# Kernel tuning notes

Measured on AMD Instinct MI355X. Metric: run time of the kernel, lower is better.

## Reference

```python
import jax, jax.numpy as jnp
import numpy as np

B, T, DM, DK, TOPK, NGRAM = 8, 4096, 1024, 256, 4, 3


def setup_inputs() -> dict:
    key = jax.random.key(0)
    k0, k1, k2, k3 = jax.random.split(key, 4)
    std = np.sqrt(2.0 / (DM + DK)).astype(np.float32)
    query = jax.random.normal(k0, (B, T, DM), jnp.float32)
    key_t = jax.random.normal(k1, (B, T, DM), jnp.float32)
    wq = jax.random.normal(k2, (DK, DM), jnp.float32) * std
    wk = jax.random.normal(k3, (DK, DM), jnp.float32) * std
    bq = jnp.zeros((DK,), jnp.float32)
    bk = jnp.zeros((DK,), jnp.float32)
    # Structured mask: each query row keeps exactly TOPK consecutive key columns
    # (required by the module's masked_select -> view(batch, -1, topk)).
    starts = np.minimum(np.arange(T), T - TOPK)
    cols = starts[:, None] + np.arange(TOPK)[None, :]  # [T, TOPK], ascending
    m = np.ones((T, T), dtype=bool)
    m[np.arange(T)[:, None], cols] = False  # False = unmasked
    mask = jnp.asarray(m)[None]  # [1, T, T]
    return {"query": query, "key": key_t, "mask": mask,
            "wq": wq, "bq": bq, "wk": wk, "bk": bk,
            "topk": TOPK, "ngram": NGRAM}


def reference(query, key, mask, wq, bq, wk, bk, topk, ngram):
    # Projections (torch Linear: x @ W.T + b)
    q = jnp.einsum('btm,dm->btd', query, wq) + bq  # [B,T,DK]
    k = jnp.einsum('btm,dm->btd', key, wk) + bk    # [B,T,DK]
    attn = jax.nn.sigmoid(jnp.einsum('btd,bsd->bts', q, k) / 256.0)  # [B,T,T]
    # masked_select of the topk unmasked entries per row, in ascending column
    # order (matches torch row-major masked_select). argsort of bool puts
    # False (unmasked) columns first, stably, i.e. in ascending column order.
    idx = jnp.argsort(mask, axis=-1)[..., :topk]           # [Bm,T,topk]
    idx = jnp.broadcast_to(idx, attn.shape[:2] + (topk,))  # [B,T,topk]
    sp = jnp.take_along_axis(attn, idx, axis=-1)           # [B,T,topk]
    Bsz = sp.shape[0]
    tt = topk * topk
    # init block: [B,topk,topk] -> repeat along new axis -> [B,1,topk,topk*topk]
    sp_init = jnp.tile(sp[:, :topk, :][:, :, None, :], (1, 1, topk, 1)).reshape(Bsz, 1, topk, tt)
    # end block: repeat each element topk times along last axis
    sp_end = jnp.tile(sp[:, -topk:, :][..., None], (1, 1, 1, topk)).reshape(Bsz, 1, topk, tt)
    # middle n-gram blocks
    mid = sp[:, topk:-topk, :].reshape(Bsz, -1, topk, ngram - 1, topk)  # [B,G,topk,2,topk]
    before = mid[:, :, :, 0, :]  # [B,G,topk,topk]
    after = mid[:, :, :, 1, :]   # [B,G,topk,topk]
    sm = jnp.einsum('bgti,bgtj->bgtij', before, after).reshape(Bsz, -1, topk, tt)
    score_matrix = jnp.concatenate([sp_init, sm, sp_end], axis=1)  # [B,G+2,topk,tt]
    return score_matrix.sum(axis=-1)  # [B, G+2, topk]
```

## Files before the change

### kernel.cpp

```cpp
#include <hip/hip_runtime.h>
#include <hip/hip_bf16.h>
#include <stdint.h>

#define B_ 8
#define T_ 4096
#define DM_ 1024
#define DK_ 256

typedef __attribute__((ext_vector_type(8))) short short8;
typedef __attribute__((ext_vector_type(4))) float f32x4;
typedef __attribute__((ext_vector_type(4))) unsigned short ushort4v;
typedef __attribute__((ext_vector_type(8))) unsigned short ushort8v;

__device__ inline float bf2f(unsigned short u) {
    union { unsigned int u; float f; } v; v.u = ((unsigned int)u) << 16; return v.f;
}
__device__ inline unsigned short f2bf(float f) {
    __hip_bfloat16 h = __float2bfloat16(f);
    return __builtin_bit_cast(unsigned short, h);
}

__device__ inline void gload_lds16(const void* g, void* l) {
    __builtin_amdgcn_global_load_lds(
        (const __attribute__((address_space(1))) unsigned int*)g,
        (__attribute__((address_space(3))) unsigned int*)l, 16, 0, 0);
}

__global__ __launch_bounds__(256) void convw_kernel(
    const float* __restrict__ Wq, const float* __restrict__ Wk,
    unsigned short* __restrict__ Wpk)
{
    int t = blockIdx.x * 256 + threadIdx.x;
    int lane = t & 63;
    int n    = (t >> 6) & 15;
    int kt   = (t >> 10) & 31;
    int M    = t >> 15;
    const float* W = M ? Wk : Wq;
    int row = n * 16 + (lane & 15);
    int k0  = kt * 32 + (lane >> 4) * 8;
    const float* src = W + (size_t)row * DM_ + k0;
    f32x4 v0 = *(const f32x4*)(src);
    f32x4 v1 = *(const f32x4*)(src + 4);
    ushort8v u;
#pragma unroll
    for (int e = 0; e < 4; ++e) { u[e] = f2bf(v0[e]); u[e + 4] = f2bf(v1[e]); }
    *(ushort8v*)(Wpk + (size_t)t * 8) = u;
}

__global__ __launch_bounds__(512, 4) void proj_kernel(
    const float* __restrict__ Aq, const float* __restrict__ Ak,
    const unsigned short* __restrict__ Wpk,
    const float* __restrict__ bq, const float* __restrict__ bk,
    unsigned short* __restrict__ Oq, unsigned short* __restrict__ Ok)
{
    __shared__ __align__(16) char smem[2][32 * 1024];

    const bool isK = (blockIdx.z != 0);
    const float* A = isK ? Ak : Aq;
    const unsigned short* Wp = Wpk + (isK ? (size_t)32 * 16 * 64 * 8 : 0);
    const float* bias = isK ? bk : bq;
    unsigned short* O = isK ? Ok : Oq;

    const int row0 = blockIdx.x * 128;
    const int tid  = threadIdx.x;
    const int w    = tid >> 6;
    const int lane = tid & 63;
    const int lr   = lane & 15;
    const int lq   = lane >> 4;
    const int wr   = (w >> 2) * 64;
    const int wc   = (w & 3);

    const int arow = lane >> 3;
    const int aslt = (lane & 7) ^ (lane >> 3);

    f32x4 acc[4][4];
#pragma unroll
    for (int m = 0; m < 4; ++m)
#pragma unroll
        for (int n = 0; n < 4; ++n) acc[m][n] = (f32x4){0.f, 0.f, 0.f, 0.f};

#define STAGE(KT, BUF) {                                               \
    char* Ab_ = smem[BUF];                                             \
    char* Wb_ = smem[BUF] + 16 * 1024;                                 \
    const unsigned short* ws_ = Wp + (size_t)(KT) * 8192 + lane * 8;   \
    _Pragma("unroll")                                                  \
    for (int i_ = 0; i_ < 2; ++i_) {                                   \
        int c_ = w * 2 + i_;                                \
        int ra_ = c_ * 8 + arow;                     \
        gload_lds16(A + (size_t)(row0 + ra_) * DM_ + (KT) * 32         \
                      + aslt * 4,                                      \
                    Ab_ + c_ * 1024);                                  \
        gload_lds16(ws_ + (size_t)c_ * 1024 / 2 * 0 + c_ * 512,        \
                    Wb_ + c_ * 1024);                                  \
    } }

    STAGE(0, 0);

    for (int kt = 0; kt < 32; ++kt) {
        const int cur = kt & 1;
        if (kt < 31) {
            STAGE(kt + 1, cur ^ 1);
            asm volatile("s_waitcnt vmcnt(4)" ::: "memory");
        } else {
            asm volatile("s_waitcnt vmcnt(0)" ::: "memory");
        }
        __builtin_amdgcn_s_barrier();

        const char* As = smem[cur];
        const char* Ws = smem[cur] + 16 * 1024;

        short8 bF[4];
#pragma unroll
        for (int n = 0; n < 4; ++n)
            bF[n] = *(const short8*)(Ws + (wc * 4 + n) * 1024 + lane * 16);

#pragma unroll
        for (int m = 0; m < 4; ++m) {
            const int r = wr + m * 16 + lr;
            f32x4 a0 = *(const f32x4*)(As + r * 128 + (((lq * 2)     ^ (r & 7)) << 4));
            f32x4 a1 = *(const f32x4*)(As + r * 128 + (((lq * 2 + 1) ^ (r & 7)) << 4));
            short8 aF;
#pragma unroll
            for (int e = 0; e < 4; ++e) {
                aF[e]     = (short)f2bf(a0[e]);
                aF[e + 4] = (short)f2bf(a1[e]);
            }
#pragma unroll
            for (int n = 0; n < 4; ++n)
                acc[m][n] = __builtin_amdgcn_mfma_f32_16x16x32_bf16(
                    bF[n], aF, acc[m][n], 0, 0, 0);
        }
        asm volatile("s_waitcnt lgkmcnt(0)" ::: "memory");
        __builtin_amdgcn_s_barrier();
    }
#undef STAGE

#pragma unroll
    for (int m = 0; m < 4; ++m) {
        unsigned short* Orow = O + (size_t)(row0 + wr + m * 16 + lr) * DK_;
#pragma unroll
        for (int n = 0; n < 4; ++n) {
            const int col = (wc * 4 + n) * 16 + lq * 4;
            f32x4 bv = *(const f32x4*)(bias + col);
            ushort4v ov;
#pragma unroll
            for (int r4 = 0; r4 < 4; ++r4) ov[r4] = f2bf(acc[m][n][r4] + bv[r4]);
            *(ushort4v*)(Orow + col) = ov;
        }
    }
}

__global__ __launch_bounds__(256) void score_kernel(
    const unsigned short* __restrict__ Q, const unsigned short* __restrict__ K,
    float* __restrict__ S)
{
    constexpr int RS = 264;
    __shared__ unsigned short qs[64 * RS];
    __shared__ unsigned short ks[68 * RS];

    const int t0  = blockIdx.x * 64;
    const int b   = blockIdx.y;
    const int tid = threadIdx.x;

#pragma unroll
    for (int j = 0; j < 8; ++j) {
        int idx = j * 256 + tid;
        int r = idx >> 5, c = idx & 31;
        ushort8v v = *(const ushort8v*)(Q + ((size_t)(b * T_ + t0 + r)) * DK_ + c * 8);
        *(ushort8v*)(qs + r * RS + c * 8) = v;
    }
#pragma unroll
    for (int j = 0; j < 9; ++j) {
        int idx = j * 256 + tid;
        if (idx < 68 * 32) {
            int r = idx >> 5, c = idx & 31;
            int gr = t0 + r; if (gr > T_ - 1) gr = T_ - 1;
            ushort8v v = *(const ushort8v*)(K + ((size_t)(b * T_ + gr)) * DK_ + c * 8);
            *(ushort8v*)(ks + r * RS + c * 8) = v;
        }
    }
    __syncthreads();

    const int tl = tid >> 2;
    const int i  = tid & 3;
    const int t  = t0 + tl;
    int s = t; if (s > T_ - 4) s = T_ - 4;
    const int kl = s - t0 + i;

    const ushort8v* qr = (const ushort8v*)(qs + tl * RS);
    const ushort8v* kr = (const ushort8v*)(ks + kl * RS);
    float acc = 0.f;
#pragma unroll
    for (int d8 = 0; d8 < 32; ++d8) {
        ushort8v a = qr[d8], bb = kr[d8];
#pragma unroll
        for (int e = 0; e < 8; ++e) acc += bf2f(a[e]) * bf2f(bb[e]);
    }
    float sig = 1.0f / (1.0f + __expf(-acc * (1.0f / 256.0f)));
    sig += __shfl_xor(sig, 1);
    sig += __shfl_xor(sig, 2);
    if (i == 0) S[(size_t)b * T_ + t] = sig;
}

__global__ void out_kernel(const float* __restrict__ S, float* __restrict__ out)
{
    int idx = blockIdx.x * 256 + threadIdx.x;
    if (idx >= B_ * 513 * 4) return;
    int r = idx & 3;
    int g = (idx >> 2) % 513;
    int b = idx / (513 * 4);
    const float* Sb = S + (size_t)b * T_;
    float v;
    if (g == 0)        v = 4.0f * Sb[r];
    else if (g == 512) v = 4.0f * Sb[T_ - 4 + r];
    else { int base = 4 + (g - 1) * 8 + r * 2; v = Sb[base] * Sb[base + 1]; }
    out[idx] = v;
}

extern "C" void kernel_launch(void* const* d_in, const int* in_sizes, int n_in,
                              void* d_out, int out_size, void* d_ws, size_t ws_size,
                              hipStream_t stream)
{
    const float* query = (const float*)d_in[0];
    const float* key   = (const float*)d_in[1];
    const float* wq = (const float*)d_in[3];
    const float* bq = (const float*)d_in[4];
    const float* wk = (const float*)d_in[5];
    const float* bk = (const float*)d_in[6];
    float* out = (float*)d_out;

    unsigned short* Qb  = (unsigned short*)d_ws;
    unsigned short* Kb  = Qb + (size_t)B_ * T_ * DK_;
    float*          Sb  = (float*)(Kb + (size_t)B_ * T_ * DK_);
    unsigned short* Wpk = (unsigned short*)(Sb + (size_t)B_ * T_);

    hipLaunchKernelGGL(convw_kernel, dim3(256), dim3(256), 0, stream, wq, wk, Wpk);

    dim3 g1(B_ * T_ / 128, 1, 2);
    hipLaunchKernelGGL(proj_kernel, g1, dim3(512), 0, stream,
                       query, key, Wpk, bq, bk, Qb, Kb);

    dim3 g2(T_ / 64, B_);
    hipLaunchKernelGGL(score_kernel, g2, dim3(256), 0, stream, Qb, Kb, Sb);

    int tot = B_ * 513 * 4;
    hipLaunchKernelGGL(out_kernel, dim3((tot + 255) / 256), dim3(256), 0, stream, Sb, out);
}
```

Measured before the change: 85.76 us.

## Split projection GEMM into 128x128 output tiles with K=64 single-buffered stages

Changes the projection kernel from 512-thread blocks covering all 256 output columns to 256-thread blocks covering 128 columns, doubling the grid along y. Each k-iteration now stages a 64-wide K slice with a 16-slot XOR swizzle and uses __syncthreads instead of double-buffering with manual waitcnt. The packed weight layout in convw is reordered to match. The aim is more blocks and occupancy with fewer iterations, but the A input is now read twice (once per column half) and load/compute overlap within a block is lost.

```diff
diff --git a/kernel.cpp b/kernel.cpp
--- a/kernel.cpp
+++ b/kernel.cpp
@@ -32,12 +32,15 @@
 {
     int t = blockIdx.x * 256 + threadIdx.x;
     int lane = t & 63;
-    int n    = (t >> 6) & 15;
-    int kt   = (t >> 10) & 31;
+    int n    = (t >> 6) & 3;
+    int w2   = (t >> 8) & 1;
+    int kk   = (t >> 9) & 1;
+    int kt   = (t >> 10) & 15;
+    int y    = (t >> 14) & 1;
     int M    = t >> 15;
     const float* W = M ? Wk : Wq;
-    int row = n * 16 + (lane & 15);
-    int k0  = kt * 32 + (lane >> 4) * 8;
+    int row = y * 128 + w2 * 64 + n * 16 + (lane & 15);
+    int k0  = kt * 64 + kk * 32 + (lane >> 4) * 8;
     const float* src = W + (size_t)row * DM_ + k0;
     f32x4 v0 = *(const f32x4*)(src);
     f32x4 v1 = *(const f32x4*)(src + 4);
@@ -47,31 +50,33 @@
     *(ushort8v*)(Wpk + (size_t)t * 8) = u;
 }
 
-__global__ __launch_bounds__(512, 4) void proj_kernel(
+__global__ __launch_bounds__(256, 3) void proj_kernel(
     const float* __restrict__ Aq, const float* __restrict__ Ak,
     const unsigned short* __restrict__ Wpk,
     const float* __restrict__ bq, const float* __restrict__ bk,
     unsigned short* __restrict__ Oq, unsigned short* __restrict__ Ok)
 {
-    __shared__ __align__(16) char smem[2][32 * 1024];
+    __shared__ __align__(16) char smem[48 * 1024];
+    char* As = smem;
+    char* Ws = smem + 32 * 1024;
 
     const bool isK = (blockIdx.z != 0);
     const float* A = isK ? Ak : Aq;
-    const unsigned short* Wp = Wpk + (isK ? (size_t)32 * 16 * 64 * 8 : 0);
+    const unsigned short* Wp = Wpk
+        + (isK ? (size_t)262144 : 0)
+        + (size_t)blockIdx.y * 131072;
     const float* bias = isK ? bk : bq;
     unsigned short* O = isK ? Ok : Oq;
 
     const int row0 = blockIdx.x * 128;
+    const int col0 = blockIdx.y * 128;
     const int tid  = threadIdx.x;
     const int w    = tid >> 6;
     const int lane = tid & 63;
     const int lr   = lane & 15;
     const int lq   = lane >> 4;
-    const int wr   = (w >> 2) * 64;
-    const int wc   = (w & 3);
-
-    const int arow = lane >> 3;
-    const int aslt = (lane & 7) ^ (lane >> 3);
+    const int wr   = (w >> 1) * 64;
+    const int wch  = (w & 1);
 
     f32x4 acc[4][4];
 #pragma unroll
@@ -79,68 +84,54 @@
 #pragma unroll
         for (int n = 0; n < 4; ++n) acc[m][n] = (f32x4){0.f, 0.f, 0.f, 0.f};
 
-#define STAGE(KT, BUF) {                                               \
-    char* Ab_ = smem[BUF];                                             \
-    char* Wb_ = smem[BUF] + 16 * 1024;                                 \
-    const unsigned short* ws_ = Wp + (size_t)(KT) * 8192 + lane * 8;   \
-    _Pragma("unroll")                                                  \
-    for (int i_ = 0; i_ < 2; ++i_) {                                   \
-        int c_ = w * 2 + i_;                                \
-        int ra_ = c_ * 8 + arow;                     \
-        gload_lds16(A + (size_t)(row0 + ra_) * DM_ + (KT) * 32         \
-                      + aslt * 4,                                      \
-                    Ab_ + c_ * 1024);                                  \
-        gload_lds16(ws_ + (size_t)c_ * 1024 / 2 * 0 + c_ * 512,        \
-                    Wb_ + c_ * 1024);                                  \
-    } }
-
-    STAGE(0, 0);
-
-    for (int kt = 0; kt < 32; ++kt) {
-        const int cur = kt & 1;
-        if (kt < 31) {
-            STAGE(kt + 1, cur ^ 1);
-            asm volatile("s_waitcnt vmcnt(4)" ::: "memory");
-        } else {
-            asm volatile("s_waitcnt vmcnt(0)" ::: "memory");
-        }
-        __builtin_amdgcn_s_barrier();
-
-        const char* As = smem[cur];
-        const char* Ws = smem[cur] + 16 * 1024;
-
-        short8 bF[4];
-#pragma unroll
-        for (int n = 0; n < 4; ++n)
-            bF[n] = *(const short8*)(Ws + (wc * 4 + n) * 1024 + lane * 16);
-
-#pragma unroll
-        for (int m = 0; m < 4; ++m) {
-            const int r = wr + m * 16 + lr;
-            f32x4 a0 = *(const f32x4*)(As + r * 128 + (((lq * 2)     ^ (r & 7)) << 4));
-            f32x4 a1 = *(const f32x4*)(As + r * 128 + (((lq * 2 + 1) ^ (r & 7)) << 4));
-            short8 aF;
-#pragma unroll
-            for (int e = 0; e < 4; ++e) {
-                aF[e]     = (short)f2bf(a0[e]);
-                aF[e + 4] = (short)f2bf(a1[e]);
+    for (int kt = 0; kt < 16; ++kt) {
+#pragma unroll
+        for (int i = 0; i < 8; ++i) {
+            int idx = i * 256 + tid;
+            int r = idx >> 4, s = idx & 15;
+            gload_lds16(A + (size_t)(row0 + r) * DM_ + kt * 64 + ((s ^ (r & 15)) << 2),
+                        As + idx * 16);
+        }
+#pragma unroll
+        for (int i = 0; i < 4; ++i) {
+            int idx = i * 256 + tid;
+            gload_lds16(Wp + (size_t)kt * 8192 + idx * 8, Ws + idx * 16);
+        }
+        __syncthreads();
+
+#pragma unroll
+        for (int kk = 0; kk < 2; ++kk) {
+            short8 bF[4];
+#pragma unroll
+            for (int n = 0; n < 4; ++n)
+                bF[n] = *(const short8*)(Ws + ((kk * 2 + wch) * 4 + n) * 1024 + lane * 16);
+#pragma unroll
+            for (int m = 0; m < 4; ++m) {
+                const int r = wr + m * 16 + lr;
+                const int sb = kk * 8 + lq * 2;
+                f32x4 a0 = *(const f32x4*)(As + r * 256 + (((sb)     ^ lr) << 4));
+                f32x4 a1 = *(const f32x4*)(As + r * 256 + (((sb + 1) ^ lr) << 4));
+                short8 aF;
+#pragma unroll
+                for (int e = 0; e < 4; ++e) {
+                    aF[e]     = (short)f2bf(a0[e]);
+                    aF[e + 4] = (short)f2bf(a1[e]);
+                }
+#pragma unroll
+                for (int n = 0; n < 4; ++n)
+                    acc[m][n] = __builtin_amdgcn_mfma_f32_16x16x32_bf16(
+                        bF[n], aF, acc[m][n], 0, 0, 0);
             }
-#pragma unroll
-            for (int n = 0; n < 4; ++n)
-                acc[m][n] = __builtin_amdgcn_mfma_f32_16x16x32_bf16(
-                    bF[n], aF, acc[m][n], 0, 0, 0);
-        }
-        asm volatile("s_waitcnt lgkmcnt(0)" ::: "memory");
-        __builtin_amdgcn_s_barrier();
-    }
-#undef STAGE
+        }
+        __syncthreads();
+    }
 
 #pragma unroll
     for (int m = 0; m < 4; ++m) {
         unsigned short* Orow = O + (size_t)(row0 + wr + m * 16 + lr) * DK_;
 #pragma unroll
         for (int n = 0; n < 4; ++n) {
-            const int col = (wc * 4 + n) * 16 + lq * 4;
+            const int col = col0 + wch * 64 + n * 16 + lq * 4;
             f32x4 bv = *(const f32x4*)(bias + col);
             ushort4v ov;
 #pragma unroll
@@ -236,8 +227,8 @@
 
     hipLaunchKernelGGL(convw_kernel, dim3(256), dim3(256), 0, stream, wq, wk, Wpk);
 
-    dim3 g1(B_ * T_ / 128, 1, 2);
-    hipLaunchKernelGGL(proj_kernel, g1, dim3(512), 0, stream,
+    dim3 g1(B_ * T_ / 128, 2, 2);
+    hipLaunchKernelGGL(proj_kernel, g1, dim3(256), 0, stream,
                        query, key, Wpk, bq, bk, Qb, Kb);
 
     dim3 g2(T_ / 64, B_);
```

Measured after the change: 102.7 us. +19.7%, slower.

## Convert A tiles to bf16 in registers before LDS and fuse output kernel

Applied to the files above, without the earlier changes.

The projection kernel now loads fp32 activations into registers, converts them to bf16 once per thread, and writes bf16 tiles to LDS. This halves the LDS footprint for A and removes the repeated per-wave conversion of the same data, while the weights keep using direct global-to-LDS loads. It also adds s_setprio around the MFMA block, lowers launch bounds occupancy to 2, and folds the output n-gram assembly into the score kernel through a shuffle, dropping one launch and the S buffer. The risk is that register-staged A loads are less latency tolerant than async LDS loads.

```diff
diff --git a/kernel.cpp b/kernel.cpp
--- a/kernel.cpp
+++ b/kernel.cpp
@@ -47,17 +47,17 @@
     *(ushort8v*)(Wpk + (size_t)t * 8) = u;
 }
 
-__global__ __launch_bounds__(512, 4) void proj_kernel(
+__global__ __launch_bounds__(512, 2) void proj_kernel(
     const float* __restrict__ Aq, const float* __restrict__ Ak,
     const unsigned short* __restrict__ Wpk,
     const float* __restrict__ bq, const float* __restrict__ bk,
     unsigned short* __restrict__ Oq, unsigned short* __restrict__ Ok)
 {
-    __shared__ __align__(16) char smem[2][32 * 1024];
+    __shared__ __align__(16) char smem[2][24576];
 
     const bool isK = (blockIdx.z != 0);
     const float* A = isK ? Ak : Aq;
-    const unsigned short* Wp = Wpk + (isK ? (size_t)32 * 16 * 64 * 8 : 0);
+    const unsigned short* Wp = Wpk + (isK ? (size_t)262144 : 0);
     const float* bias = isK ? bk : bq;
     unsigned short* O = isK ? Ok : Oq;
 
@@ -68,10 +68,12 @@
     const int lr   = lane & 15;
     const int lq   = lane >> 4;
     const int wr   = (w >> 2) * 64;
-    const int wc   = (w & 3);
-
-    const int arow = lane >> 3;
-    const int aslt = (lane & 7) ^ (lane >> 3);
+    const int wc   = w & 3;
+
+    const int srow = tid >> 2;
+    const int schk = tid & 3;
+    const float* Asrc = A + (size_t)(row0 + srow) * DM_ + schk * 8;
+    const int awaddr = srow * 64 + ((schk ^ (srow & 3)) << 4);
 
     f32x4 acc[4][4];
 #pragma unroll
@@ -79,61 +81,60 @@
 #pragma unroll
         for (int n = 0; n < 4; ++n) acc[m][n] = (f32x4){0.f, 0.f, 0.f, 0.f};
 
-#define STAGE(KT, BUF) {                                               \
-    char* Ab_ = smem[BUF];                                             \
-    char* Wb_ = smem[BUF] + 16 * 1024;                                 \
-    const unsigned short* ws_ = Wp + (size_t)(KT) * 8192 + lane * 8;   \
-    _Pragma("unroll")                                                  \
-    for (int i_ = 0; i_ < 2; ++i_) {                                   \
-        int c_ = w * 2 + i_;                                \
-        int ra_ = c_ * 8 + arow;                     \
-        gload_lds16(A + (size_t)(row0 + ra_) * DM_ + (KT) * 32         \
-                      + aslt * 4,                                      \
-                    Ab_ + c_ * 1024);                                  \
-        gload_lds16(ws_ + (size_t)c_ * 1024 / 2 * 0 + c_ * 512,        \
-                    Wb_ + c_ * 1024);                                  \
-    } }
-
-    STAGE(0, 0);
+    f32x4 av0, av1;
+
+#define LOADA(KT) { const float* p_ = Asrc + (KT) * 32;            \
+                    av0 = *(const f32x4*)(p_);                      \
+                    av1 = *(const f32x4*)(p_ + 4); }
+#define STAGEW(KT, BUF) {                                           \
+    const unsigned short* ws_ = Wp + (size_t)(KT) * 8192;           \
+    gload_lds16(ws_ + (size_t)tid * 8,          smem[BUF] + 8192  + tid * 16); \
+    gload_lds16(ws_ + (size_t)(tid + 512) * 8,  smem[BUF] + 16384 + tid * 16); }
+#define CVTWRITE(BUF) {                                             \
+    ushort8v u_;                                                    \
+    _Pragma("unroll")                                               \
+    for (int e_ = 0; e_ < 4; ++e_) {                                \
+        u_[e_]     = f2bf(av0[e_]);                                 \
+        u_[e_ + 4] = f2bf(av1[e_]);                                 \
+    }                                                               \
+    *(ushort8v*)(smem[BUF] + awaddr) = u_; }
+
+    STAGEW(0, 0);
+    LOADA(0);
+    CVTWRITE(0);
+    __syncthreads();
 
     for (int kt = 0; kt < 32; ++kt) {
         const int cur = kt & 1;
         if (kt < 31) {
-            STAGE(kt + 1, cur ^ 1);
-            asm volatile("s_waitcnt vmcnt(4)" ::: "memory");
-        } else {
-            asm volatile("s_waitcnt vmcnt(0)" ::: "memory");
-        }
-        __builtin_amdgcn_s_barrier();
+            STAGEW(kt + 1, cur ^ 1);
+            LOADA(kt + 1);
+        }
 
         const char* As = smem[cur];
-        const char* Ws = smem[cur] + 16 * 1024;
-
+        const char* Ws = smem[cur] + 8192;
+        __builtin_amdgcn_s_setprio(1);
         short8 bF[4];
 #pragma unroll
         for (int n = 0; n < 4; ++n)
-            bF[n] = *(const short8*)(Ws + (wc * 4 + n) * 1024 + lane * 16);
-
+            bF[n] = *(const short8*)(Ws + ((wc * 4 + n) << 10) + (lane << 4));
 #pragma unroll
         for (int m = 0; m < 4; ++m) {
             const int r = wr + m * 16 + lr;
-            f32x4 a0 = *(const f32x4*)(As + r * 128 + (((lq * 2)     ^ (r & 7)) << 4));
-            f32x4 a1 = *(const f32x4*)(As + r * 128 + (((lq * 2 + 1) ^ (r & 7)) << 4));
-            short8 aF;
-#pragma unroll
-            for (int e = 0; e < 4; ++e) {
-                aF[e]     = (short)f2bf(a0[e]);
-                aF[e + 4] = (short)f2bf(a1[e]);
-            }
+            short8 aF = *(const short8*)(As + r * 64 + ((lq ^ (lr & 3)) << 4));
 #pragma unroll
             for (int n = 0; n < 4; ++n)
                 acc[m][n] = __builtin_amdgcn_mfma_f32_16x16x32_bf16(
                     bF[n], aF, acc[m][n], 0, 0, 0);
         }
-        asm volatile("s_waitcnt lgkmcnt(0)" ::: "memory");
-        __builtin_amdgcn_s_barrier();
-    }
-#undef STAGE
+        __builtin_amdgcn_s_setprio(0);
+
+        if (kt < 31) CVTWRITE(cur ^ 1);
+        __syncthreads();
+    }
+#undef LOADA
+#undef STAGEW
+#undef CVTWRITE
 
 #pragma unroll
     for (int m = 0; m < 4; ++m) {
@@ -152,7 +153,7 @@
 
 __global__ __launch_bounds__(256) void score_kernel(
     const unsigned short* __restrict__ Q, const unsigned short* __restrict__ K,
-    float* __restrict__ S)
+    float* __restrict__ out)
 {
     constexpr int RS = 264;
     __shared__ unsigned short qs[64 * RS];
@@ -199,22 +200,22 @@
     float sig = 1.0f / (1.0f + __expf(-acc * (1.0f / 256.0f)));
     sig += __shfl_xor(sig, 1);
     sig += __shfl_xor(sig, 2);
-    if (i == 0) S[(size_t)b * T_ + t] = sig;
-}
-
-__global__ void out_kernel(const float* __restrict__ S, float* __restrict__ out)
-{
-    int idx = blockIdx.x * 256 + threadIdx.x;
-    if (idx >= B_ * 513 * 4) return;
-    int r = idx & 3;
-    int g = (idx >> 2) % 513;
-    int b = idx / (513 * 4);
-    const float* Sb = S + (size_t)b * T_;
-    float v;
-    if (g == 0)        v = 4.0f * Sb[r];
-    else if (g == 512) v = 4.0f * Sb[T_ - 4 + r];
-    else { int base = 4 + (g - 1) * 8 + r * 2; v = Sb[base] * Sb[base + 1]; }
-    out[idx] = v;
+    float Snext = __shfl_xor(sig, 4);
+
+    if (i == 0) {
+        float* ob = out + (size_t)b * (513 * 4);
+        if (t < 4) {
+            ob[t] = 4.0f * sig;
+        } else if (t >= T_ - 4) {
+            ob[512 * 4 + (t - (T_ - 4))] = 4.0f * sig;
+        }
+        if ((t & 1) == 0 && t >= 4 && t < T_ - 4) {
+            int pos = t - 4;
+            int g = (pos >> 3) + 1;
+            int r = (pos >> 1) & 3;
+            ob[g * 4 + r] = sig * Snext;
+        }
+    }
 }
 
 extern "C" void kernel_launch(void* const* d_in, const int* in_sizes, int n_in,
@@ -231,8 +232,7 @@
 
     unsigned short* Qb  = (unsigned short*)d_ws;
     unsigned short* Kb  = Qb + (size_t)B_ * T_ * DK_;
-    float*          Sb  = (float*)(Kb + (size_t)B_ * T_ * DK_);
-    unsigned short* Wpk = (unsigned short*)(Sb + (size_t)B_ * T_);
+    unsigned short* Wpk = Kb + (size_t)B_ * T_ * DK_;
 
     hipLaunchKernelGGL(convw_kernel, dim3(256), dim3(256), 0, stream, wq, wk, Wpk);
 
@@ -241,8 +241,5 @@
                        query, key, Wpk, bq, bk, Qb, Kb);
 
     dim3 g2(T_ / 64, B_);
-    hipLaunchKernelGGL(score_kernel, g2, dim3(256), 0, stream, Qb, Kb, Sb);
-
-    int tot = B_ * 513 * 4;
-    hipLaunchKernelGGL(out_kernel, dim3((tot + 255) / 256), dim3(256), 0, stream, Sb, out);
-}
+    hipLaunchKernelGGL(score_kernel, g2, dim3(256), 0, stream, Qb, Kb, out);
+}
```

Measured after the change: 85.84 us. Within noise of the previous version (+0.1%).
